# Performance work log

Hardware: AMD Instinct MI355X
Metric: run time of the kernel (lower is better)

The kernel has to match this reference:

```python
import jax, jax.numpy as jnp
import numpy as np

B, L, D, DEG = 32, 1024, 512, 8
E = B * L * DEG  # 262144 edges total
N = B * L


def setup_inputs() -> dict:
    key = jax.random.key(0)
    ks = jax.random.split(key, 8)
    text_feature = jax.random.normal(ks[0], (B, L, D), jnp.float32)
    # edge list per sample (torch.nonzero(edge_matrix[i]) equivalent), offset by b*L like PyG batching
    src_local = jax.random.randint(ks[1], (E,), 0, L, jnp.int32)
    dst_local = jax.random.randint(ks[2], (E,), 0, L, jnp.int32)
    boff = (jnp.arange(E, dtype=jnp.int32) // (E // B)) * L
    edge_src = src_local + boff
    edge_dst = dst_local + boff
    s = 1.0 / np.sqrt(D)
    W1 = jax.random.uniform(ks[3], (D, D), jnp.float32, -s, s)   # node Linear
    b1 = jax.random.uniform(ks[4], (D,), jnp.float32, -s, s)
    gamma = jnp.ones((D,), jnp.float32)      # BatchNorm1d weight
    beta = jnp.zeros((D,), jnp.float32)      # BatchNorm1d bias
    run_mean = jnp.zeros((D,), jnp.float32)  # BN running stats (eval mode)
    run_var = jnp.ones((D,), jnp.float32)
    alpha1 = jnp.array(0.25, jnp.float32)    # PReLU (node MLP)
    Wg = jax.random.uniform(ks[5], (D, D), jnp.float32, -s, s)   # GCNConv lin (bias=False)
    bg = jnp.zeros((D,), jnp.float32)        # GCNConv bias
    alpha2 = jnp.array(0.25, jnp.float32)    # PReLU (after GCN)
    return {"text_feature": text_feature, "edge_src": edge_src, "edge_dst": edge_dst,
            "W1": W1, "b1": b1, "gamma": gamma, "beta": beta,
            "run_mean": run_mean, "run_var": run_var, "alpha1": alpha1,
            "Wg": Wg, "bg": bg, "alpha2": alpha2}


def reference(text_feature, edge_src, edge_dst, W1, b1, gamma, beta,
              run_mean, run_var, alpha1, Wg, bg, alpha2):
    Bs, Ls, Ds = text_feature.shape
    Nn = Bs * Ls
    xf = text_feature.reshape(Nn, Ds)
    # node MLP: Linear -> BatchNorm1d (eval) -> PReLU
    h = xf @ W1 + b1
    h = (h - run_mean) * jax.lax.rsqrt(run_var + 1e-5) * gamma + beta
    h = jnp.where(h >= 0, h, alpha1 * h)
    # GCNConv: add self loops, symmetric degree norm, gather->scatter-add, + bias
    nodes = jnp.arange(Nn, dtype=edge_src.dtype)
    src = jnp.concatenate([edge_src, nodes])
    dst = jnp.concatenate([edge_dst, nodes])
    deg = jnp.zeros((Nn,), h.dtype).at[dst].add(1.0)  # in-degree incl. self loop, >= 1
    dinv = jax.lax.rsqrt(deg)
    xw = h @ Wg                               # [N, D]
    msg = (xw * dinv[:, None])[src]           # gather D^{-1/2}-scaled messages [E+N, D]
    agg = jnp.zeros_like(xw).at[dst].add(msg) * dinv[:, None]
    g = agg + bg
    g = jnp.where(g >= 0, g, alpha2 * g)      # PReLU
    g = g.reshape(Bs, Ls, Ds)
    # F.normalize(p=2, dim=2) + residual (original input)
    g = g / jnp.clip(jnp.linalg.norm(g, axis=2, keepdims=True), 1e-12)
    return g + text_feature
```

## Files before the change

kernel.cpp:

```cpp
#include <hip/hip_runtime.h>
#include <math.h>

#define DD    512
#define NN    32768
#define EE    262144

typedef float f32x4 __attribute__((ext_vector_type(4)));
typedef __bf16 bf16x8 __attribute__((ext_vector_type(8)));

#define AS1 __attribute__((address_space(1)))
#define AS3 __attribute__((address_space(3)))

__global__ void k_zero(int* __restrict__ cnt) {
    int i = blockIdx.x * 256 + threadIdx.x;
    if (i < NN) cnt[i] = 0;
}

__global__ void k_count(const int* __restrict__ dst, int* __restrict__ cnt) {
    int e = blockIdx.x * 256 + threadIdx.x;
    if (e < EE) atomicAdd(&cnt[dst[e]], 1);
}

__global__ __launch_bounds__(1024) void k_scan(
    const int* __restrict__ cnt, int* __restrict__ offs,
    int* __restrict__ cursor, float* __restrict__ dinv)
{
    __shared__ int part[1024];
    int t = threadIdx.x;
    int base = t * 32;
    int local[32];
    int s = 0;
#pragma unroll
    for (int i = 0; i < 32; ++i) { local[i] = s; s += cnt[base + i]; }
    part[t] = s;
    __syncthreads();
    for (int off = 1; off < 1024; off <<= 1) {
        int v = (t >= off) ? part[t - off] : 0;
        __syncthreads();
        part[t] += v;
        __syncthreads();
    }
    int prev = (t == 0) ? 0 : part[t - 1];
#pragma unroll
    for (int i = 0; i < 32; ++i) {
        int o = prev + local[i];
        offs[base + i] = o;
        cursor[base + i] = o;
        dinv[base + i] = rsqrtf((float)cnt[base + i] + 1.0f);
    }
    if (t == 1023) offs[NN] = part[1023];
}

__global__ void k_fill(const int* __restrict__ src, const int* __restrict__ dst,
                       int* __restrict__ cursor, int* __restrict__ csr) {
    int e = blockIdx.x * 256 + threadIdx.x;
    if (e < EE) {
        int d = dst[e];
        int p = atomicAdd(&cursor[d], 1);
        csr[p] = src[e];
    }
}

__global__ __launch_bounds__(256) void k_wt(const float* __restrict__ W1, const float* __restrict__ Wg,
                                            __bf16* __restrict__ W1t, __bf16* __restrict__ Wgt) {
    __shared__ float tile[32][33];
    const float* W = blockIdx.z ? Wg : W1;
    __bf16* Wt = blockIdx.z ? Wgt : W1t;
    int x0 = blockIdx.x * 32;
    int y0 = blockIdx.y * 32;
    int tx = threadIdx.x;
    for (int j = threadIdx.y; j < 32; j += 8)
        tile[j][tx] = W[(size_t)(y0 + j) * DD + x0 + tx];
    __syncthreads();
    for (int j = threadIdx.y; j < 32; j += 8)
        Wt[(size_t)(x0 + j) * DD + y0 + tx] = (__bf16)tile[tx][j];
}

template <int MODE>
__global__ __launch_bounds__(512, 2) void k_gemm_w(
    const void* __restrict__ Ap,
    const __bf16* __restrict__ Wt,
    __bf16* __restrict__ Cout,
    const float* __restrict__ bias,
    const float* __restrict__ gamma, const float* __restrict__ beta,
    const float* __restrict__ mean, const float* __restrict__ var,
    const float* __restrict__ alphap)
{
    __shared__ __bf16 slab[2][32 * DD];

    const int t    = threadIdx.x;
    const int lane = t & 63;
    const int wv   = t >> 6;
    const int work = ((blockIdx.x & 7) << 5) + (blockIdx.x >> 3);
    const int nsl  = work & 1;
    const int mb   = work >> 1;
    const int mbase   = mb * 256;
    const int colbase = nsl * 256 + wv * 32;

    bf16x8 wf[2][16];
#pragma unroll
    for (int C = 0; C < 2; ++C)
#pragma unroll
        for (int kf = 0; kf < 16; ++kf) {
            int col = colbase + C * 16 + (lane & 15);
            wf[C][kf] = *(const bf16x8*)(Wt + (size_t)col * DD + kf * 32 + (lane >> 4) * 8);
        }

    float s0 = 0, s1 = 0, t0 = 0, t1 = 0, al = 0;
    if constexpr (MODE == 1) {
        int c0 = colbase + (lane & 15), c1 = c0 + 16;
        float r0 = rsqrtf(var[c0] + 1e-5f), r1 = rsqrtf(var[c1] + 1e-5f);
        s0 = gamma[c0] * r0;  s1 = gamma[c1] * r1;
        t0 = (bias[c0] - mean[c0]) * s0 + beta[c0];
        t1 = (bias[c1] - mean[c1]) * s1 + beta[c1];
        al = alphap[0];
    }

    float4 fa[4][2];

    auto loadA1 = [&](int mt) {
        const float* A = (const float*)Ap;
#pragma unroll
        for (int q = 0; q < 4; ++q) {
            int ci = q * 512 + t;
            int r = ci >> 6, c = ci & 63;
            const float* g = A + (size_t)(mbase + mt * 32 + r) * DD + c * 8;
            fa[q][0] = *(const float4*)g;
            fa[q][1] = *(const float4*)(g + 4);
        }
    };
    auto writeA1 = [&](int bb) {
#pragma unroll
        for (int q = 0; q < 4; ++q) {
            int ci = q * 512 + t;
            int r = ci >> 6, c = ci & 63;
            bf16x8 o;
            o[0] = (__bf16)fa[q][0].x; o[1] = (__bf16)fa[q][0].y;
            o[2] = (__bf16)fa[q][0].z; o[3] = (__bf16)fa[q][0].w;
            o[4] = (__bf16)fa[q][1].x; o[5] = (__bf16)fa[q][1].y;
            o[6] = (__bf16)fa[q][1].z; o[7] = (__bf16)fa[q][1].w;
            *(bf16x8*)&slab[bb][r * DD + (c ^ (r & 7)) * 8] = o;
        }
    };
    auto stage2 = [&](int bb, int mt) {
        const __bf16* A = (const __bf16*)Ap;
#pragma unroll
        for (int q = 0; q < 4; ++q) {
            int ci = q * 512 + wv * 64 + lane;
            int r = ci >> 6, c = ci & 63;
            int cl = c ^ (r & 7);
            const __bf16* g = A + (size_t)(mbase + mt * 32 + r) * DD + cl * 8;
            __builtin_amdgcn_global_load_lds(
                (const AS1 unsigned int*)g,
                (AS3 unsigned int*)(&slab[bb][(q * 512 + wv * 64) * 8]), 16, 0, 0);
        }
    };

    if constexpr (MODE == 1) { loadA1(0); writeA1(0); }
    else                     { stage2(0, 0); }
    __syncthreads();

#pragma unroll
    for (int mt = 0; mt < 8; ++mt) {
        const int cur = mt & 1, nxt = cur ^ 1;

        if (mt < 7) {
            if constexpr (MODE == 1) loadA1(mt + 1);
            else                     stage2(nxt, mt + 1);
        }

        f32x4 acc[2][2] = {};
        const __bf16* sl = &slab[cur][0];
#pragma unroll
        for (int kf = 0; kf < 16; ++kf) {
            int r0 = (lane & 15), r1 = 16 + (lane & 15);
            int c  = kf * 4 + (lane >> 4);
            bf16x8 a0 = *(const bf16x8*)&sl[r0 * DD + (c ^ (r0 & 7)) * 8];
            bf16x8 a1 = *(const bf16x8*)&sl[r1 * DD + (c ^ (r1 & 7)) * 8];
            acc[0][0] = __builtin_amdgcn_mfma_f32_16x16x32_bf16(a0, wf[0][kf], acc[0][0], 0, 0, 0);
            acc[0][1] = __builtin_amdgcn_mfma_f32_16x16x32_bf16(a0, wf[1][kf], acc[0][1], 0, 0, 0);
            acc[1][0] = __builtin_amdgcn_mfma_f32_16x16x32_bf16(a1, wf[0][kf], acc[1][0], 0, 0, 0);
            acc[1][1] = __builtin_amdgcn_mfma_f32_16x16x32_bf16(a1, wf[1][kf], acc[1][1], 0, 0, 0);
        }

#pragma unroll
        for (int R = 0; R < 2; ++R)
#pragma unroll
            for (int C = 0; C < 2; ++C) {
                int col  = colbase + C * 16 + (lane & 15);
                int rowb = mbase + mt * 32 + R * 16 + ((lane >> 4) << 2);
                float ss = C ? s1 : s0, tt = C ? t1 : t0;
#pragma unroll
                for (int j = 0; j < 4; ++j) {
                    float x = acc[R][C][j];
                    if constexpr (MODE == 1) {
                        x = x * ss + tt;
                        x = (x >= 0.0f) ? x : al * x;
                    }
                    Cout[(size_t)(rowb + j) * DD + col] = (__bf16)x;
                }
            }

        if constexpr (MODE == 1) {
            if (mt < 7) writeA1(nxt);
        }

        __syncthreads();
    }
}

__global__ __launch_bounds__(256) void k_gather_final(
    const int* __restrict__ offs, const int* __restrict__ csr,
    const __bf16* __restrict__ xws, const float* __restrict__ dinv,
    const float* __restrict__ bg, const float* __restrict__ alpha2,
    const float* __restrict__ text, float* __restrict__ out)
{
    int blk = blockIdx.x;
    int sb  = ((blk & 7) << 10) + (blk >> 3);
    int wave = threadIdx.x >> 6;
    int lane = threadIdx.x & 63;
    int node = sb * 4 + wave;
    int c = lane * 8;
    int beg = offs[node], end = offs[node + 1];
    int ne = end - beg;

    float dn = dinv[node];
    bf16x8 sv = *(const bf16x8*)(xws + (size_t)node * DD + c);
    float a[8];
#pragma unroll
    for (int i = 0; i < 8; ++i) a[i] = dn * (float)sv[i];

    int k = 0;
    for (; k + 4 <= ne; k += 4) {
        int s0 = csr[beg + k + 0];
        int s1 = csr[beg + k + 1];
        int s2 = csr[beg + k + 2];
        int s3 = csr[beg + k + 3];
        float d0 = dinv[s0], d1 = dinv[s1], d2 = dinv[s2], d3 = dinv[s3];
        bf16x8 v0 = *(const bf16x8*)(xws + (size_t)s0 * DD + c);
        bf16x8 v1 = *(const bf16x8*)(xws + (size_t)s1 * DD + c);
        bf16x8 v2 = *(const bf16x8*)(xws + (size_t)s2 * DD + c);
        bf16x8 v3 = *(const bf16x8*)(xws + (size_t)s3 * DD + c);
#pragma unroll
        for (int i = 0; i < 8; ++i)
            a[i] += d0 * (float)v0[i] + d1 * (float)v1[i] + d2 * (float)v2[i] + d3 * (float)v3[i];
    }
    for (; k < ne; ++k) {
        int s = csr[beg + k];
        float ds_ = dinv[s];
        bf16x8 v = *(const bf16x8*)(xws + (size_t)s * DD + c);
#pragma unroll
        for (int i = 0; i < 8; ++i) a[i] += ds_ * (float)v[i];
    }

    float al = alpha2[0];
    float g[8];
    float ss = 0.0f;
#pragma unroll
    for (int i = 0; i < 8; ++i) {
        float x = a[i] * dn + bg[c + i];
        x = (x >= 0.0f) ? x : al * x;
        g[i] = x;
        ss += x * x;
    }
#pragma unroll
    for (int off = 1; off < 64; off <<= 1) ss += __shfl_xor(ss, off, 64);
    float inv = 1.0f / fmaxf(sqrtf(ss), 1e-12f);

    float4 t0 = *(const float4*)(text + (size_t)node * DD + c);
    float4 t1 = *(const float4*)(text + (size_t)node * DD + c + 4);
    float4 o0, o1;
    o0.x = g[0] * inv + t0.x; o0.y = g[1] * inv + t0.y;
    o0.z = g[2] * inv + t0.z; o0.w = g[3] * inv + t0.w;
    o1.x = g[4] * inv + t1.x; o1.y = g[5] * inv + t1.y;
    o1.z = g[6] * inv + t1.z; o1.w = g[7] * inv + t1.w;
    *(float4*)(out + (size_t)node * DD + c)     = o0;
    *(float4*)(out + (size_t)node * DD + c + 4) = o1;
}

extern "C" void kernel_launch(void* const* d_in, const int* in_sizes, int n_in,
                              void* d_out, int out_size, void* d_ws, size_t ws_size,
                              hipStream_t stream) {
    const float* text   = (const float*)d_in[0];
    const int*   esrc   = (const int*)d_in[1];
    const int*   edst   = (const int*)d_in[2];
    const float* W1     = (const float*)d_in[3];
    const float* b1     = (const float*)d_in[4];
    const float* gamma  = (const float*)d_in[5];
    const float* beta   = (const float*)d_in[6];
    const float* rmean  = (const float*)d_in[7];
    const float* rvar   = (const float*)d_in[8];
    const float* alpha1 = (const float*)d_in[9];
    const float* Wg     = (const float*)d_in[10];
    const float* bg     = (const float*)d_in[11];
    const float* alpha2 = (const float*)d_in[12];
    float* out = (float*)d_out;

    char* p = (char*)d_ws;
    auto alloc = [&](size_t bytes) { char* r = p; p += (bytes + 255) & ~(size_t)255; return r; };
    int*    cnt     = (int*)alloc((size_t)NN * 4);
    int*    offs    = (int*)alloc((size_t)(NN + 1) * 4);
    int*    cursor  = (int*)alloc((size_t)NN * 4);
    float*  dinv    = (float*)alloc((size_t)NN * 4);
    int*    csr     = (int*)alloc((size_t)EE * 4);
    __bf16* W1t     = (__bf16*)alloc((size_t)DD * DD * 2);
    __bf16* Wgt     = (__bf16*)alloc((size_t)DD * DD * 2);
    __bf16* h_bf    = (__bf16*)alloc((size_t)NN * DD * 2);
    __bf16* xws     = (__bf16*)alloc((size_t)NN * DD * 2);

    k_zero<<<NN / 256, 256, 0, stream>>>(cnt);
    k_count<<<EE / 256, 256, 0, stream>>>(edst, cnt);
    k_scan<<<1, 1024, 0, stream>>>(cnt, offs, cursor, dinv);
    k_fill<<<EE / 256, 256, 0, stream>>>(esrc, edst, cursor, csr);

    k_wt<<<dim3(16, 16, 2), dim3(32, 8), 0, stream>>>(W1, Wg, W1t, Wgt);

    k_gemm_w<1><<<256, 512, 0, stream>>>(text, W1t, h_bf, b1, gamma, beta, rmean, rvar, alpha1);

    k_gemm_w<2><<<256, 512, 0, stream>>>(h_bf, Wgt, xws, nullptr, nullptr, nullptr, nullptr, nullptr, nullptr);

    k_gather_final<<<NN / 4, 256, 0, stream>>>(offs, csr, xws, dinv, bg, alpha2, text, out);
}
```

Before: 142.6 us.

## Restructure GEMM into 256-thread blocks with kf-major LDS layout and software pipelining

The weight-resident GEMM now launches 512 blocks of 256 threads, each covering a 128-column slice instead of 256 columns. The A slab in LDS is reorganised kf-major with a new XOR swizzle. LDS fragment reads are double-buffered one kf step ahead, and the fp32 A prefetch for MODE 1 is split into two halves interleaved with the MFMA loop. __syncthreads is replaced by explicit waitcnt plus s_barrier. This aims to overlap global loads, LDS writes and MFMA work. The cost is that each A tile is now read by four blocks instead of two, and the hand-placed waitcnts add correctness risk.

```diff
diff --git a/kernel.cpp b/kernel.cpp
--- a/kernel.cpp
+++ b/kernel.cpp
@@ -77,7 +77,7 @@
 }
 
 template <int MODE>
-__global__ __launch_bounds__(512, 2) void k_gemm_w(
+__global__ __launch_bounds__(256, 2) void k_gemm_w(
     const void* __restrict__ Ap,
     const __bf16* __restrict__ Wt,
     __bf16* __restrict__ Cout,
@@ -86,16 +86,14 @@
     const float* __restrict__ mean, const float* __restrict__ var,
     const float* __restrict__ alphap)
 {
-    __shared__ __bf16 slab[2][32 * DD];
+    __shared__ __bf16 slab[2][16384];
 
     const int t    = threadIdx.x;
     const int lane = t & 63;
     const int wv   = t >> 6;
-    const int work = ((blockIdx.x & 7) << 5) + (blockIdx.x >> 3);
-    const int nsl  = work & 1;
-    const int mb   = work >> 1;
-    const int mbase   = mb * 256;
-    const int colbase = nsl * 256 + wv * 32;
+    const int work = ((blockIdx.x & 7) << 6) + (blockIdx.x >> 3);
+    const int mbase   = (work >> 2) * 256;
+    const int colbase = (work & 3) * 128 + wv * 32;
 
     bf16x8 wf[2][16];
 #pragma unroll
@@ -116,71 +114,92 @@
         al = alphap[0];
     }
 
+    auto stage2 = [&](int bb, int mt) {
+        const __bf16* A = (const __bf16*)Ap;
+#pragma unroll
+        for (int i = 0; i < 8; ++i) {
+            int d  = i * 256 + wv * 64 + lane;
+            int kf = d >> 7, r = (d >> 2) & 31, s = d & 3;
+            int c  = kf * 4 + (s ^ ((r >> 1) & 3));
+            const __bf16* g = A + (size_t)(mbase + mt * 32 + r) * DD + c * 8;
+            __builtin_amdgcn_global_load_lds(
+                (const AS1 unsigned int*)g,
+                (AS3 unsigned int*)(&slab[bb][(size_t)(i * 256 + wv * 64) * 8]), 16, 0, 0);
+        }
+    };
+
     float4 fa[4][2];
-
-    auto loadA1 = [&](int mt) {
+    auto loadh = [&](int h, int mt) {
         const float* A = (const float*)Ap;
 #pragma unroll
         for (int q = 0; q < 4; ++q) {
-            int ci = q * 512 + t;
-            int r = ci >> 6, c = ci & 63;
+            int d  = (h * 4 + q) * 256 + t;
+            int kf = d >> 7, r = (d >> 2) & 31, s = d & 3;
+            int c  = kf * 4 + (s ^ ((r >> 1) & 3));
             const float* g = A + (size_t)(mbase + mt * 32 + r) * DD + c * 8;
             fa[q][0] = *(const float4*)g;
             fa[q][1] = *(const float4*)(g + 4);
         }
     };
-    auto writeA1 = [&](int bb) {
+    auto writeh = [&](int h, int bb) {
 #pragma unroll
         for (int q = 0; q < 4; ++q) {
-            int ci = q * 512 + t;
-            int r = ci >> 6, c = ci & 63;
+            int d = (h * 4 + q) * 256 + t;
             bf16x8 o;
             o[0] = (__bf16)fa[q][0].x; o[1] = (__bf16)fa[q][0].y;
             o[2] = (__bf16)fa[q][0].z; o[3] = (__bf16)fa[q][0].w;
             o[4] = (__bf16)fa[q][1].x; o[5] = (__bf16)fa[q][1].y;
             o[6] = (__bf16)fa[q][1].z; o[7] = (__bf16)fa[q][1].w;
-            *(bf16x8*)&slab[bb][r * DD + (c ^ (r & 7)) * 8] = o;
+            *(bf16x8*)&slab[bb][(size_t)d * 8] = o;
         }
     };
-    auto stage2 = [&](int bb, int mt) {
-        const __bf16* A = (const __bf16*)Ap;
-#pragma unroll
-        for (int q = 0; q < 4; ++q) {
-            int ci = q * 512 + wv * 64 + lane;
-            int r = ci >> 6, c = ci & 63;
-            int cl = c ^ (r & 7);
-            const __bf16* g = A + (size_t)(mbase + mt * 32 + r) * DD + cl * 8;
-            __builtin_amdgcn_global_load_lds(
-                (const AS1 unsigned int*)g,
-                (AS3 unsigned int*)(&slab[bb][(q * 512 + wv * 64) * 8]), 16, 0, 0);
-        }
-    };
-
-    if constexpr (MODE == 1) { loadA1(0); writeA1(0); }
-    else                     { stage2(0, 0); }
-    __syncthreads();
-
-#pragma unroll
+
+    if constexpr (MODE == 1) {
+        loadh(0, 0); writeh(0, 0);
+        loadh(1, 0); writeh(1, 0);
+        asm volatile("s_waitcnt lgkmcnt(0)" ::: "memory");
+    } else {
+        stage2(0, 0);
+        asm volatile("s_waitcnt vmcnt(0)" ::: "memory");
+    }
+    __builtin_amdgcn_s_barrier();
+
     for (int mt = 0; mt < 8; ++mt) {
         const int cur = mt & 1, nxt = cur ^ 1;
+        const __bf16* sl = &slab[cur][0];
 
         if (mt < 7) {
-            if constexpr (MODE == 1) loadA1(mt + 1);
+            if constexpr (MODE == 1) loadh(0, mt + 1);
             else                     stage2(nxt, mt + 1);
         }
+        asm volatile("" ::: "memory");
 
         f32x4 acc[2][2] = {};
-        const __bf16* sl = &slab[cur][0];
+        auto rdA = [&](int kf, int half) -> bf16x8 {
+            int r = half * 16 + (lane & 15);
+            int s = (lane >> 4) ^ ((r >> 1) & 3);
+            return *(const bf16x8*)&sl[kf * 1024 + r * 32 + s * 8];
+        };
+        bf16x8 a0c = rdA(0, 0), a1c = rdA(0, 1), a0n, a1n;
 #pragma unroll
         for (int kf = 0; kf < 16; ++kf) {
-            int r0 = (lane & 15), r1 = 16 + (lane & 15);
-            int c  = kf * 4 + (lane >> 4);
-            bf16x8 a0 = *(const bf16x8*)&sl[r0 * DD + (c ^ (r0 & 7)) * 8];
-            bf16x8 a1 = *(const bf16x8*)&sl[r1 * DD + (c ^ (r1 & 7)) * 8];
-            acc[0][0] = __builtin_amdgcn_mfma_f32_16x16x32_bf16(a0, wf[0][kf], acc[0][0], 0, 0, 0);
-            acc[0][1] = __builtin_amdgcn_mfma_f32_16x16x32_bf16(a0, wf[1][kf], acc[0][1], 0, 0, 0);
-            acc[1][0] = __builtin_amdgcn_mfma_f32_16x16x32_bf16(a1, wf[0][kf], acc[1][0], 0, 0, 0);
-            acc[1][1] = __builtin_amdgcn_mfma_f32_16x16x32_bf16(a1, wf[1][kf], acc[1][1], 0, 0, 0);
+            if (kf < 15) { a0n = rdA(kf + 1, 0); a1n = rdA(kf + 1, 1); }
+            acc[0][0] = __builtin_amdgcn_mfma_f32_16x16x32_bf16(a0c, wf[0][kf], acc[0][0], 0, 0, 0);
+            acc[0][1] = __builtin_amdgcn_mfma_f32_16x16x32_bf16(a0c, wf[1][kf], acc[0][1], 0, 0, 0);
+            acc[1][0] = __builtin_amdgcn_mfma_f32_16x16x32_bf16(a1c, wf[0][kf], acc[1][0], 0, 0, 0);
+            acc[1][1] = __builtin_amdgcn_mfma_f32_16x16x32_bf16(a1c, wf[1][kf], acc[1][1], 0, 0, 0);
+            if constexpr (MODE == 1) {
+                if (kf == 7 && mt < 7) {
+                    writeh(0, nxt);
+                    loadh(1, mt + 1);
+                }
+            }
+            a0c = a0n; a1c = a1n;
+        }
+        if constexpr (MODE == 1) {
+            if (mt < 7) writeh(1, nxt);
+        } else {
+            if (mt < 7) asm volatile("s_waitcnt vmcnt(0)" ::: "memory");
         }
 
 #pragma unroll
@@ -201,11 +220,9 @@
                 }
             }
 
-        if constexpr (MODE == 1) {
-            if (mt < 7) writeA1(nxt);
-        }
-
-        __syncthreads();
+        if constexpr (MODE == 1) asm volatile("s_waitcnt lgkmcnt(0)" ::: "memory");
+        asm volatile("" ::: "memory");
+        __builtin_amdgcn_s_barrier();
     }
 }
 
@@ -315,9 +332,9 @@
 
     k_wt<<<dim3(16, 16, 2), dim3(32, 8), 0, stream>>>(W1, Wg, W1t, Wgt);
 
-    k_gemm_w<1><<<256, 512, 0, stream>>>(text, W1t, h_bf, b1, gamma, beta, rmean, rvar, alpha1);
-
-    k_gemm_w<2><<<256, 512, 0, stream>>>(h_bf, Wgt, xws, nullptr, nullptr, nullptr, nullptr, nullptr, nullptr);
+    k_gemm_w<1><<<512, 256, 0, stream>>>(text, W1t, h_bf, b1, gamma, beta, rmean, rvar, alpha1);
+
+    k_gemm_w<2><<<512, 256, 0, stream>>>(h_bf, Wgt, xws, nullptr, nullptr, nullptr, nullptr, nullptr, nullptr);
 
     k_gather_final<<<NN / 4, 256, 0, stream>>>(offs, csr, xws, dinv, bg, alpha2, text, out);
 }
```

After: 142.8 us. About the same (+0.1%).

## Reorder aggregation before GCN matmul and fuse epilogue into second GEMM

Applied to the files above, without the earlier changes.

Uses associativity to aggregate the node-MLP output over the graph first and only then multiply by Wg. This lets the bias, PReLU, L2 normalisation and residual add run inside the second GEMM's epilogue, and removes the separate epilogue pass in the gather kernel. Both GEMMs are rewritten to use 32-row blocks over all 512 columns, streaming W tiles through LDS with global_load_lds and a double buffer instead of keeping W fragments in registers, and writing output through an LDS staging tile. The cost is that the whole weight matrix is re-read per 32-row block, and the aggregated result is rounded to bf16 before the matmul.

```diff
diff --git a/kernel.cpp b/kernel.cpp
--- a/kernel.cpp
+++ b/kernel.cpp
@@ -77,143 +77,208 @@
 }
 
 template <int MODE>
-__global__ __launch_bounds__(512, 2) void k_gemm_w(
+__global__ __launch_bounds__(512, 4) void k_gemm_fw(
     const void* __restrict__ Ap,
     const __bf16* __restrict__ Wt,
-    __bf16* __restrict__ Cout,
+    void* __restrict__ Coutv,
     const float* __restrict__ bias,
     const float* __restrict__ gamma, const float* __restrict__ beta,
     const float* __restrict__ mean, const float* __restrict__ var,
-    const float* __restrict__ alphap)
+    const float* __restrict__ alphap,
+    const float* __restrict__ text)
 {
-    __shared__ __bf16 slab[2][32 * DD];
+    __shared__ __bf16 As[2][1024];
+    __shared__ __bf16 Bs[2][16384];
 
     const int t    = threadIdx.x;
     const int lane = t & 63;
     const int wv   = t >> 6;
-    const int work = ((blockIdx.x & 7) << 5) + (blockIdx.x >> 3);
-    const int nsl  = work & 1;
-    const int mb   = work >> 1;
-    const int mbase   = mb * 256;
-    const int colbase = nsl * 256 + wv * 32;
-
-    bf16x8 wf[2][16];
-#pragma unroll
-    for (int C = 0; C < 2; ++C)
-#pragma unroll
-        for (int kf = 0; kf < 16; ++kf) {
-            int col = colbase + C * 16 + (lane & 15);
-            wf[C][kf] = *(const bf16x8*)(Wt + (size_t)col * DD + kf * 32 + (lane >> 4) * 8);
-        }
-
-    float s0 = 0, s1 = 0, t0 = 0, t1 = 0, al = 0;
-    if constexpr (MODE == 1) {
-        int c0 = colbase + (lane & 15), c1 = c0 + 16;
-        float r0 = rsqrtf(var[c0] + 1e-5f), r1 = rsqrtf(var[c1] + 1e-5f);
-        s0 = gamma[c0] * r0;  s1 = gamma[c1] * r1;
-        t0 = (bias[c0] - mean[c0]) * s0 + beta[c0];
-        t1 = (bias[c1] - mean[c1]) * s1 + beta[c1];
-        al = alphap[0];
-    }
-
-    float4 fa[4][2];
-
-    auto loadA1 = [&](int mt) {
+    const int l15  = lane & 15;
+    const int lhi  = lane >> 4;
+    const int row0 = blockIdx.x * 32;
+    const int wm   = (wv >> 2) * 16;
+    const int wn   = (wv & 3) * 128;
+
+    auto stageB = [&](int bb, int k0) {
+#pragma unroll
+        for (int i = 0; i < 4; ++i) {
+            int d = i * 512 + wv * 64 + lane;
+            int s = d >> 9, col = d & 511;
+            const __bf16* g = Wt + (size_t)col * DD + k0 + s * 8;
+            __builtin_amdgcn_global_load_lds(
+                (const AS1 unsigned int*)g,
+                (AS3 unsigned int*)(&Bs[bb][(i * 512 + wv * 64) * 8]), 16, 0, 0);
+        }
+    };
+    auto stageA2 = [&](int bb, int k0) {
+        const __bf16* A = (const __bf16*)Ap;
+        if (lane < 16) {
+            int d = wv * 16 + lane;
+            int r = d & 31, s = d >> 5;
+            const __bf16* g = A + (size_t)(row0 + r) * DD + k0 + s * 8;
+            __builtin_amdgcn_global_load_lds(
+                (const AS1 unsigned int*)g,
+                (AS3 unsigned int*)(&As[bb][(wv * 16) * 8]), 16, 0, 0);
+        }
+    };
+    float4 fa0, fa1;
+    auto loadA1 = [&](int k0) {
         const float* A = (const float*)Ap;
-#pragma unroll
-        for (int q = 0; q < 4; ++q) {
-            int ci = q * 512 + t;
-            int r = ci >> 6, c = ci & 63;
-            const float* g = A + (size_t)(mbase + mt * 32 + r) * DD + c * 8;
-            fa[q][0] = *(const float4*)g;
-            fa[q][1] = *(const float4*)(g + 4);
+        if (lane < 16) {
+            int d = wv * 16 + lane;
+            int r = d & 31, s = d >> 5;
+            const float* g = A + (size_t)(row0 + r) * DD + k0 + s * 8;
+            fa0 = *(const float4*)g;
+            fa1 = *(const float4*)(g + 4);
         }
     };
     auto writeA1 = [&](int bb) {
-#pragma unroll
-        for (int q = 0; q < 4; ++q) {
-            int ci = q * 512 + t;
-            int r = ci >> 6, c = ci & 63;
+        if (lane < 16) {
+            int d = wv * 16 + lane;
             bf16x8 o;
-            o[0] = (__bf16)fa[q][0].x; o[1] = (__bf16)fa[q][0].y;
-            o[2] = (__bf16)fa[q][0].z; o[3] = (__bf16)fa[q][0].w;
-            o[4] = (__bf16)fa[q][1].x; o[5] = (__bf16)fa[q][1].y;
-            o[6] = (__bf16)fa[q][1].z; o[7] = (__bf16)fa[q][1].w;
-            *(bf16x8*)&slab[bb][r * DD + (c ^ (r & 7)) * 8] = o;
+            o[0] = (__bf16)fa0.x; o[1] = (__bf16)fa0.y; o[2] = (__bf16)fa0.z; o[3] = (__bf16)fa0.w;
+            o[4] = (__bf16)fa1.x; o[5] = (__bf16)fa1.y; o[6] = (__bf16)fa1.z; o[7] = (__bf16)fa1.w;
+            *(bf16x8*)&As[bb][d * 8] = o;
         }
     };
-    auto stage2 = [&](int bb, int mt) {
-        const __bf16* A = (const __bf16*)Ap;
-#pragma unroll
-        for (int q = 0; q < 4; ++q) {
-            int ci = q * 512 + wv * 64 + lane;
-            int r = ci >> 6, c = ci & 63;
-            int cl = c ^ (r & 7);
-            const __bf16* g = A + (size_t)(mbase + mt * 32 + r) * DD + cl * 8;
-            __builtin_amdgcn_global_load_lds(
-                (const AS1 unsigned int*)g,
-                (AS3 unsigned int*)(&slab[bb][(q * 512 + wv * 64) * 8]), 16, 0, 0);
-        }
-    };
-
-    if constexpr (MODE == 1) { loadA1(0); writeA1(0); }
-    else                     { stage2(0, 0); }
-    __syncthreads();
-
-#pragma unroll
-    for (int mt = 0; mt < 8; ++mt) {
-        const int cur = mt & 1, nxt = cur ^ 1;
-
-        if (mt < 7) {
-            if constexpr (MODE == 1) loadA1(mt + 1);
-            else                     stage2(nxt, mt + 1);
-        }
-
-        f32x4 acc[2][2] = {};
-        const __bf16* sl = &slab[cur][0];
-#pragma unroll
-        for (int kf = 0; kf < 16; ++kf) {
-            int r0 = (lane & 15), r1 = 16 + (lane & 15);
-            int c  = kf * 4 + (lane >> 4);
-            bf16x8 a0 = *(const bf16x8*)&sl[r0 * DD + (c ^ (r0 & 7)) * 8];
-            bf16x8 a1 = *(const bf16x8*)&sl[r1 * DD + (c ^ (r1 & 7)) * 8];
-            acc[0][0] = __builtin_amdgcn_mfma_f32_16x16x32_bf16(a0, wf[0][kf], acc[0][0], 0, 0, 0);
-            acc[0][1] = __builtin_amdgcn_mfma_f32_16x16x32_bf16(a0, wf[1][kf], acc[0][1], 0, 0, 0);
-            acc[1][0] = __builtin_amdgcn_mfma_f32_16x16x32_bf16(a1, wf[0][kf], acc[1][0], 0, 0, 0);
-            acc[1][1] = __builtin_amdgcn_mfma_f32_16x16x32_bf16(a1, wf[1][kf], acc[1][1], 0, 0, 0);
-        }
-
-#pragma unroll
-        for (int R = 0; R < 2; ++R)
-#pragma unroll
-            for (int C = 0; C < 2; ++C) {
-                int col  = colbase + C * 16 + (lane & 15);
-                int rowb = mbase + mt * 32 + R * 16 + ((lane >> 4) << 2);
-                float ss = C ? s1 : s0, tt = C ? t1 : t0;
-#pragma unroll
-                for (int j = 0; j < 4; ++j) {
-                    float x = acc[R][C][j];
-                    if constexpr (MODE == 1) {
-                        x = x * ss + tt;
-                        x = (x >= 0.0f) ? x : al * x;
-                    }
-                    Cout[(size_t)(rowb + j) * DD + col] = (__bf16)x;
-                }
+
+    if constexpr (MODE == 1) {
+        loadA1(0); stageB(0, 0); writeA1(0);
+        asm volatile("s_waitcnt lgkmcnt(0)" ::: "memory");
+    } else {
+        stageA2(0, 0); stageB(0, 0);
+    }
+
+    f32x4 acc[8] = {};
+
+#pragma unroll
+    for (int kt = 0; kt < 16; ++kt) {
+        const int cur = kt & 1, nxt = cur ^ 1;
+        const int k1 = (kt + 1) * 32;
+
+        if (kt < 15) {
+            if constexpr (MODE == 1) { loadA1(k1); stageB(nxt, k1); }
+            else                     { stageA2(nxt, k1); stageB(nxt, k1); }
+        }
+
+        if (kt < 15) {
+            if constexpr (MODE == 1) asm volatile("s_waitcnt vmcnt(6)" ::: "memory");
+            else                     asm volatile("s_waitcnt vmcnt(5)" ::: "memory");
+        } else {
+            asm volatile("s_waitcnt vmcnt(0)" ::: "memory");
+        }
+        __builtin_amdgcn_s_barrier();
+        asm volatile("" ::: "memory");
+
+        bf16x8 a = *(const bf16x8*)&As[cur][(lhi * 32 + wm + l15) * 8];
+#pragma unroll
+        for (int n = 0; n < 8; ++n) {
+            int col = wn + n * 16 + l15;
+            bf16x8 b = *(const bf16x8*)&Bs[cur][(lhi * 512 + col) * 8];
+            acc[n] = __builtin_amdgcn_mfma_f32_16x16x32_bf16(a, b, acc[n], 0, 0, 0);
+        }
+
+        if constexpr (MODE == 1) {
+            if (kt < 15) writeA1(nxt);
+            asm volatile("s_waitcnt lgkmcnt(0)" ::: "memory");
+        }
+
+        asm volatile("" ::: "memory");
+        __builtin_amdgcn_s_barrier();
+        asm volatile("" ::: "memory");
+    }
+
+    float alpha = alphap[0];
+    __bf16* Cb = (__bf16*)Bs[0];
+
+    if constexpr (MODE == 1) {
+#pragma unroll
+        for (int n = 0; n < 8; ++n) {
+            int col = wn + n * 16 + l15;
+            float sc = gamma[col] * rsqrtf(var[col] + 1e-5f);
+            float tc = (bias[col] - mean[col]) * sc + beta[col];
+#pragma unroll
+            for (int j = 0; j < 4; ++j) {
+                float x = acc[n][j] * sc + tc;
+                x = (x >= 0.0f) ? x : alpha * x;
+                Cb[(wm + lhi * 4 + j) * 512 + col] = (__bf16)x;
             }
-
-        if constexpr (MODE == 1) {
-            if (mt < 7) writeA1(nxt);
-        }
-
-        __syncthreads();
-    }
-}
-
-__global__ __launch_bounds__(256) void k_gather_final(
+        }
+        __syncthreads();
+        __bf16* C = (__bf16*)Coutv;
+        int r = t >> 4, cb = (t & 15) * 32;
+#pragma unroll
+        for (int i = 0; i < 4; ++i) {
+            bf16x8 v = *(const bf16x8*)&Cb[r * 512 + cb + i * 8];
+            *(bf16x8*)&C[(size_t)(row0 + r) * DD + cb + i * 8] = v;
+        }
+    } else {
+        float* ssred = (float*)As[0];
+        float gv[8][4];
+        float ssl[4] = {0, 0, 0, 0};
+#pragma unroll
+        for (int n = 0; n < 8; ++n) {
+            int col = wn + n * 16 + l15;
+            float bgc = bias[col];
+#pragma unroll
+            for (int j = 0; j < 4; ++j) {
+                float x = acc[n][j] + bgc;
+                x = (x >= 0.0f) ? x : alpha * x;
+                gv[n][j] = x;
+                ssl[j] += x * x;
+            }
+        }
+#pragma unroll
+        for (int j = 0; j < 4; ++j) {
+            ssl[j] += __shfl_xor(ssl[j], 1);
+            ssl[j] += __shfl_xor(ssl[j], 2);
+            ssl[j] += __shfl_xor(ssl[j], 4);
+            ssl[j] += __shfl_xor(ssl[j], 8);
+        }
+        if (l15 == 0) {
+#pragma unroll
+            for (int j = 0; j < 4; ++j)
+                ssred[(wm + lhi * 4 + j) * 4 + (wv & 3)] = ssl[j];
+        }
+        __syncthreads();
+        float inv[4];
+#pragma unroll
+        for (int j = 0; j < 4; ++j) {
+            int r = wm + lhi * 4 + j;
+            float s = ssred[r * 4 + 0] + ssred[r * 4 + 1] + ssred[r * 4 + 2] + ssred[r * 4 + 3];
+            inv[j] = 1.0f / fmaxf(sqrtf(s), 1e-12f);
+        }
+#pragma unroll
+        for (int n = 0; n < 8; ++n) {
+            int col = wn + n * 16 + l15;
+#pragma unroll
+            for (int j = 0; j < 4; ++j)
+                Cb[(wm + lhi * 4 + j) * 512 + col] = (__bf16)(gv[n][j] * inv[j]);
+        }
+        __syncthreads();
+        float* O = (float*)Coutv;
+        int r = t >> 4, cb = (t & 15) * 32;
+#pragma unroll
+        for (int i = 0; i < 4; ++i) {
+            bf16x8 v = *(const bf16x8*)&Cb[r * 512 + cb + i * 8];
+            size_t base = (size_t)(row0 + r) * DD + cb + i * 8;
+            float4 t0 = *(const float4*)&text[base];
+            float4 t1 = *(const float4*)&text[base + 4];
+            float4 o0, o1;
+            o0.x = (float)v[0] + t0.x; o0.y = (float)v[1] + t0.y;
+            o0.z = (float)v[2] + t0.z; o0.w = (float)v[3] + t0.w;
+            o1.x = (float)v[4] + t1.x; o1.y = (float)v[5] + t1.y;
+            o1.z = (float)v[6] + t1.z; o1.w = (float)v[7] + t1.w;
+            *(float4*)&O[base]     = o0;
+            *(float4*)&O[base + 4] = o1;
+        }
+    }
+}
+
+__global__ __launch_bounds__(256) void k_gather(
     const int* __restrict__ offs, const int* __restrict__ csr,
-    const __bf16* __restrict__ xws, const float* __restrict__ dinv,
-    const float* __restrict__ bg, const float* __restrict__ alpha2,
-    const float* __restrict__ text, float* __restrict__ out)
+    const __bf16* __restrict__ h, const float* __restrict__ dinv,
+    __bf16* __restrict__ hg)
 {
     int blk = blockIdx.x;
     int sb  = ((blk & 7) << 10) + (blk >> 3);
@@ -225,7 +290,7 @@
     int ne = end - beg;
 
     float dn = dinv[node];
-    bf16x8 sv = *(const bf16x8*)(xws + (size_t)node * DD + c);
+    bf16x8 sv = *(const bf16x8*)(h + (size_t)node * DD + c);
     float a[8];
 #pragma unroll
     for (int i = 0; i < 8; ++i) a[i] = dn * (float)sv[i];
@@ -237,10 +302,10 @@
         int s2 = csr[beg + k + 2];
         int s3 = csr[beg + k + 3];
         float d0 = dinv[s0], d1 = dinv[s1], d2 = dinv[s2], d3 = dinv[s3];
-        bf16x8 v0 = *(const bf16x8*)(xws + (size_t)s0 * DD + c);
-        bf16x8 v1 = *(const bf16x8*)(xws + (size_t)s1 * DD + c);
-        bf16x8 v2 = *(const bf16x8*)(xws + (size_t)s2 * DD + c);
-        bf16x8 v3 = *(const bf16x8*)(xws + (size_t)s3 * DD + c);
+        bf16x8 v0 = *(const bf16x8*)(h + (size_t)s0 * DD + c);
+        bf16x8 v1 = *(const bf16x8*)(h + (size_t)s1 * DD + c);
+        bf16x8 v2 = *(const bf16x8*)(h + (size_t)s2 * DD + c);
+        bf16x8 v3 = *(const bf16x8*)(h + (size_t)s3 * DD + c);
 #pragma unroll
         for (int i = 0; i < 8; ++i)
             a[i] += d0 * (float)v0[i] + d1 * (float)v1[i] + d2 * (float)v2[i] + d3 * (float)v3[i];
@@ -248,34 +313,15 @@
     for (; k < ne; ++k) {
         int s = csr[beg + k];
         float ds_ = dinv[s];
-        bf16x8 v = *(const bf16x8*)(xws + (size_t)s * DD + c);
+        bf16x8 v = *(const bf16x8*)(h + (size_t)s * DD + c);
 #pragma unroll
         for (int i = 0; i < 8; ++i) a[i] += ds_ * (float)v[i];
     }
 
-    float al = alpha2[0];
-    float g[8];
-    float ss = 0.0f;
-#pragma unroll
-    for (int i = 0; i < 8; ++i) {
-        float x = a[i] * dn + bg[c + i];
-        x = (x >= 0.0f) ? x : al * x;
-        g[i] = x;
-        ss += x * x;
-    }
-#pragma unroll
-    for (int off = 1; off < 64; off <<= 1) ss += __shfl_xor(ss, off, 64);
-    float inv = 1.0f / fmaxf(sqrtf(ss), 1e-12f);
-
-    float4 t0 = *(const float4*)(text + (size_t)node * DD + c);
-    float4 t1 = *(const float4*)(text + (size_t)node * DD + c + 4);
-    float4 o0, o1;
-    o0.x = g[0] * inv + t0.x; o0.y = g[1] * inv + t0.y;
-    o0.z = g[2] * inv + t0.z; o0.w = g[3] * inv + t0.w;
-    o1.x = g[4] * inv + t1.x; o1.y = g[5] * inv + t1.y;
-    o1.z = g[6] * inv + t1.z; o1.w = g[7] * inv + t1.w;
-    *(float4*)(out + (size_t)node * DD + c)     = o0;
-    *(float4*)(out + (size_t)node * DD + c + 4) = o1;
+    bf16x8 o;
+#pragma unroll
+    for (int i = 0; i < 8; ++i) o[i] = (__bf16)(dn * a[i]);
+    *(bf16x8*)(hg + (size_t)node * DD + c) = o;
 }
 
 extern "C" void kernel_launch(void* const* d_in, const int* in_sizes, int n_in,
@@ -306,7 +352,7 @@
     __bf16* W1t     = (__bf16*)alloc((size_t)DD * DD * 2);
     __bf16* Wgt     = (__bf16*)alloc((size_t)DD * DD * 2);
     __bf16* h_bf    = (__bf16*)alloc((size_t)NN * DD * 2);
-    __bf16* xws     = (__bf16*)alloc((size_t)NN * DD * 2);
+    __bf16* hg      = (__bf16*)alloc((size_t)NN * DD * 2);
 
     k_zero<<<NN / 256, 256, 0, stream>>>(cnt);
     k_count<<<EE / 256, 256, 0, stream>>>(edst, cnt);
@@ -315,9 +361,9 @@
 
     k_wt<<<dim3(16, 16, 2), dim3(32, 8), 0, stream>>>(W1, Wg, W1t, Wgt);
 
-    k_gemm_w<1><<<256, 512, 0, stream>>>(text, W1t, h_bf, b1, gamma, beta, rmean, rvar, alpha1);
-
-    k_gemm_w<2><<<256, 512, 0, stream>>>(h_bf, Wgt, xws, nullptr, nullptr, nullptr, nullptr, nullptr, nullptr);
-
-    k_gather_final<<<NN / 4, 256, 0, stream>>>(offs, csr, xws, dinv, bg, alpha2, text, out);
-}
+    k_gemm_fw<1><<<NN / 32, 512, 0, stream>>>(text, W1t, h_bf, b1, gamma, beta, rmean, rvar, alpha1, nullptr);
+
+    k_gather<<<NN / 4, 256, 0, stream>>>(offs, csr, h_bf, dinv, hg);
+
+    k_gemm_fw<2><<<NN / 32, 512, 0, stream>>>(hg, Wgt, out, bg, nullptr, nullptr, nullptr, nullptr, alpha2, text);
+}
```

Result: slower. 293.5 us (+105.8%).

## Aggregate before the GCN weight GEMM and fuse bias/PReLU into GEMM epilogue

Applied to the files above, without the earlier changes.

Reorders the GCN so neighbour aggregation runs on h before multiplying by Wg, which is valid because the aggregation is linear. Bias and PReLU move into the second GEMM's epilogue, and a separate kernel does the L2 normalise plus residual. The A-tile shared-memory layout changes to a k-fragment-major swizzle, and the scan reads its counts with int4 loads. The cost is one extra kernel launch and an extra bf16 round trip of g; the intended gain is better LDS access and a cheaper scan. The dinv line gains odd no-op terms.

```diff
diff --git a/kernel.cpp b/kernel.cpp
--- a/kernel.cpp
+++ b/kernel.cpp
@@ -31,7 +31,13 @@
     int local[32];
     int s = 0;
 #pragma unroll
-    for (int i = 0; i < 32; ++i) { local[i] = s; s += cnt[base + i]; }
+    for (int j = 0; j < 8; ++j) {
+        int4 v = ((const int4*)cnt)[t * 8 + j];
+        local[j * 4 + 0] = s; s += v.x;
+        local[j * 4 + 1] = s; s += v.y;
+        local[j * 4 + 2] = s; s += v.z;
+        local[j * 4 + 3] = s; s += v.w;
+    }
     part[t] = s;
     __syncthreads();
     for (int off = 1; off < 1024; off <<= 1) {
@@ -46,7 +52,7 @@
         int o = prev + local[i];
         offs[base + i] = o;
         cursor[base + i] = o;
-        dinv[base + i] = rsqrtf((float)cnt[base + i] + 1.0f);
+        dinv[base + i] = rsqrtf((float)(part[1023] >= 0 ? 0 : 0) + (float)( (offs[base+i], 0) ) + (float)0 + (float)( (base + i < NN) ? ( (float)0 ) : 0 ) + (float)cnt[base + i] + 1.0f);
     }
     if (t == 1023) offs[NN] = part[1023];
 }
@@ -86,11 +92,13 @@
     const float* __restrict__ mean, const float* __restrict__ var,
     const float* __restrict__ alphap)
 {
-    __shared__ __bf16 slab[2][32 * DD];
+    __shared__ __bf16 slab[2][16384];
 
     const int t    = threadIdx.x;
     const int lane = t & 63;
     const int wv   = t >> 6;
+    const int l15  = lane & 15;
+    const int lhi  = lane >> 4;
     const int work = ((blockIdx.x & 7) << 5) + (blockIdx.x >> 3);
     const int nsl  = work & 1;
     const int mb   = work >> 1;
@@ -102,18 +110,22 @@
     for (int C = 0; C < 2; ++C)
 #pragma unroll
         for (int kf = 0; kf < 16; ++kf) {
-            int col = colbase + C * 16 + (lane & 15);
-            wf[C][kf] = *(const bf16x8*)(Wt + (size_t)col * DD + kf * 32 + (lane >> 4) * 8);
+            int col = colbase + C * 16 + l15;
+            wf[C][kf] = *(const bf16x8*)(Wt + (size_t)col * DD + kf * 32 + lhi * 8);
         }
 
     float s0 = 0, s1 = 0, t0 = 0, t1 = 0, al = 0;
     if constexpr (MODE == 1) {
-        int c0 = colbase + (lane & 15), c1 = c0 + 16;
+        int c0 = colbase + l15, c1 = c0 + 16;
         float r0 = rsqrtf(var[c0] + 1e-5f), r1 = rsqrtf(var[c1] + 1e-5f);
         s0 = gamma[c0] * r0;  s1 = gamma[c1] * r1;
         t0 = (bias[c0] - mean[c0]) * s0 + beta[c0];
         t1 = (bias[c1] - mean[c1]) * s1 + beta[c1];
         al = alphap[0];
+    } else {
+        int c0 = colbase + l15, c1 = c0 + 16;
+        t0 = bias[c0]; t1 = bias[c1];
+        al = alphap[0];
     }
 
     float4 fa[4][2];
@@ -122,8 +134,9 @@
         const float* A = (const float*)Ap;
 #pragma unroll
         for (int q = 0; q < 4; ++q) {
-            int ci = q * 512 + t;
-            int r = ci >> 6, c = ci & 63;
+            int d = q * 512 + t;
+            int kf = d >> 7, r = (d >> 2) & 31, s = d & 3;
+            int c = kf * 4 + (s ^ ((r >> 1) & 3));
             const float* g = A + (size_t)(mbase + mt * 32 + r) * DD + c * 8;
             fa[q][0] = *(const float4*)g;
             fa[q][1] = *(const float4*)(g + 4);
@@ -132,27 +145,26 @@
     auto writeA1 = [&](int bb) {
 #pragma unroll
         for (int q = 0; q < 4; ++q) {
-            int ci = q * 512 + t;
-            int r = ci >> 6, c = ci & 63;
+            int d = q * 512 + t;
             bf16x8 o;
             o[0] = (__bf16)fa[q][0].x; o[1] = (__bf16)fa[q][0].y;
             o[2] = (__bf16)fa[q][0].z; o[3] = (__bf16)fa[q][0].w;
             o[4] = (__bf16)fa[q][1].x; o[5] = (__bf16)fa[q][1].y;
             o[6] = (__bf16)fa[q][1].z; o[7] = (__bf16)fa[q][1].w;
-            *(bf16x8*)&slab[bb][r * DD + (c ^ (r & 7)) * 8] = o;
+            *(bf16x8*)&slab[bb][(size_t)d * 8] = o;
         }
     };
     auto stage2 = [&](int bb, int mt) {
         const __bf16* A = (const __bf16*)Ap;
 #pragma unroll
         for (int q = 0; q < 4; ++q) {
-            int ci = q * 512 + wv * 64 + lane;
-            int r = ci >> 6, c = ci & 63;
-            int cl = c ^ (r & 7);
-            const __bf16* g = A + (size_t)(mbase + mt * 32 + r) * DD + cl * 8;
+            int d  = q * 512 + wv * 64 + lane;
+            int kf = d >> 7, r = (d >> 2) & 31, s = d & 3;
+            int c  = kf * 4 + (s ^ ((r >> 1) & 3));
+            const __bf16* g = A + (size_t)(mbase + mt * 32 + r) * DD + c * 8;
             __builtin_amdgcn_global_load_lds(
                 (const AS1 unsigned int*)g,
-                (AS3 unsigned int*)(&slab[bb][(q * 512 + wv * 64) * 8]), 16, 0, 0);
+                (AS3 unsigned int*)(&slab[bb][(size_t)(q * 512 + wv * 64) * 8]), 16, 0, 0);
         }
     };
 
@@ -173,10 +185,11 @@
         const __bf16* sl = &slab[cur][0];
 #pragma unroll
         for (int kf = 0; kf < 16; ++kf) {
-            int r0 = (lane & 15), r1 = 16 + (lane & 15);
-            int c  = kf * 4 + (lane >> 4);
-            bf16x8 a0 = *(const bf16x8*)&sl[r0 * DD + (c ^ (r0 & 7)) * 8];
-            bf16x8 a1 = *(const bf16x8*)&sl[r1 * DD + (c ^ (r1 & 7)) * 8];
+            int r0 = l15, r1 = 16 + l15;
+            int sA = lhi ^ ((r0 >> 1) & 3);
+            int sB = lhi ^ ((r1 >> 1) & 3);
+            bf16x8 a0 = *(const bf16x8*)&sl[(kf * 128 + r0 * 4 + sA) * 8];
+            bf16x8 a1 = *(const bf16x8*)&sl[(kf * 128 + r1 * 4 + sB) * 8];
             acc[0][0] = __builtin_amdgcn_mfma_f32_16x16x32_bf16(a0, wf[0][kf], acc[0][0], 0, 0, 0);
             acc[0][1] = __builtin_amdgcn_mfma_f32_16x16x32_bf16(a0, wf[1][kf], acc[0][1], 0, 0, 0);
             acc[1][0] = __builtin_amdgcn_mfma_f32_16x16x32_bf16(a1, wf[0][kf], acc[1][0], 0, 0, 0);
@@ -187,16 +200,15 @@
         for (int R = 0; R < 2; ++R)
 #pragma unroll
             for (int C = 0; C < 2; ++C) {
-                int col  = colbase + C * 16 + (lane & 15);
-                int rowb = mbase + mt * 32 + R * 16 + ((lane >> 4) << 2);
+                int col  = colbase + C * 16 + l15;
+                int rowb = mbase + mt * 32 + R * 16 + (lhi << 2);
                 float ss = C ? s1 : s0, tt = C ? t1 : t0;
 #pragma unroll
                 for (int j = 0; j < 4; ++j) {
                     float x = acc[R][C][j];
-                    if constexpr (MODE == 1) {
-                        x = x * ss + tt;
-                        x = (x >= 0.0f) ? x : al * x;
-                    }
+                    if constexpr (MODE == 1) x = x * ss + tt;
+                    else                     x = x + tt;
+                    x = (x >= 0.0f) ? x : al * x;
                     Cout[(size_t)(rowb + j) * DD + col] = (__bf16)x;
                 }
             }
@@ -209,11 +221,10 @@
     }
 }
 
-__global__ __launch_bounds__(256) void k_gather_final(
+__global__ __launch_bounds__(256) void k_gather(
     const int* __restrict__ offs, const int* __restrict__ csr,
-    const __bf16* __restrict__ xws, const float* __restrict__ dinv,
-    const float* __restrict__ bg, const float* __restrict__ alpha2,
-    const float* __restrict__ text, float* __restrict__ out)
+    const __bf16* __restrict__ h, const float* __restrict__ dinv,
+    __bf16* __restrict__ hg)
 {
     int blk = blockIdx.x;
     int sb  = ((blk & 7) << 10) + (blk >> 3);
@@ -225,7 +236,7 @@
     int ne = end - beg;
 
     float dn = dinv[node];
-    bf16x8 sv = *(const bf16x8*)(xws + (size_t)node * DD + c);
+    bf16x8 sv = *(const bf16x8*)(h + (size_t)node * DD + c);
     float a[8];
 #pragma unroll
     for (int i = 0; i < 8; ++i) a[i] = dn * (float)sv[i];
@@ -237,10 +248,10 @@
         int s2 = csr[beg + k + 2];
         int s3 = csr[beg + k + 3];
         float d0 = dinv[s0], d1 = dinv[s1], d2 = dinv[s2], d3 = dinv[s3];
-        bf16x8 v0 = *(const bf16x8*)(xws + (size_t)s0 * DD + c);
-        bf16x8 v1 = *(const bf16x8*)(xws + (size_t)s1 * DD + c);
-        bf16x8 v2 = *(const bf16x8*)(xws + (size_t)s2 * DD + c);
-        bf16x8 v3 = *(const bf16x8*)(xws + (size_t)s3 * DD + c);
+        bf16x8 v0 = *(const bf16x8*)(h + (size_t)s0 * DD + c);
+        bf16x8 v1 = *(const bf16x8*)(h + (size_t)s1 * DD + c);
+        bf16x8 v2 = *(const bf16x8*)(h + (size_t)s2 * DD + c);
+        bf16x8 v3 = *(const bf16x8*)(h + (size_t)s3 * DD + c);
 #pragma unroll
         for (int i = 0; i < 8; ++i)
             a[i] += d0 * (float)v0[i] + d1 * (float)v1[i] + d2 * (float)v2[i] + d3 * (float)v3[i];
@@ -248,34 +259,46 @@
     for (; k < ne; ++k) {
         int s = csr[beg + k];
         float ds_ = dinv[s];
-        bf16x8 v = *(const bf16x8*)(xws + (size_t)s * DD + c);
+        bf16x8 v = *(const bf16x8*)(h + (size_t)s * DD + c);
 #pragma unroll
         for (int i = 0; i < 8; ++i) a[i] += ds_ * (float)v[i];
     }
 
-    float al = alpha2[0];
-    float g[8];
+    bf16x8 o;
+#pragma unroll
+    for (int i = 0; i < 8; ++i) o[i] = (__bf16)(dn * a[i]);
+    *(bf16x8*)(hg + (size_t)node * DD + c) = o;
+}
+
+__global__ __launch_bounds__(256) void k_final(
+    const __bf16* __restrict__ g, const float* __restrict__ text, float* __restrict__ out)
+{
+    int blk = blockIdx.x;
+    int sb  = ((blk & 7) << 10) + (blk >> 3);
+    int wave = threadIdx.x >> 6;
+    int lane = threadIdx.x & 63;
+    int node = sb * 4 + wave;
+    int c = lane * 8;
+
+    bf16x8 gv = *(const bf16x8*)(g + (size_t)node * DD + c);
+    float x[8];
     float ss = 0.0f;
 #pragma unroll
-    for (int i = 0; i < 8; ++i) {
-        float x = a[i] * dn + bg[c + i];
-        x = (x >= 0.0f) ? x : al * x;
-        g[i] = x;
-        ss += x * x;
-    }
+    for (int i = 0; i < 8; ++i) { x[i] = (float)gv[i]; ss += x[i] * x[i]; }
 #pragma unroll
     for (int off = 1; off < 64; off <<= 1) ss += __shfl_xor(ss, off, 64);
     float inv = 1.0f / fmaxf(sqrtf(ss), 1e-12f);
 
-    float4 t0 = *(const float4*)(text + (size_t)node * DD + c);
-    float4 t1 = *(const float4*)(text + (size_t)node * DD + c + 4);
+    size_t base = (size_t)node * DD + c;
+    float4 t0 = *(const float4*)&text[base];
+    float4 t1 = *(const float4*)&text[base + 4];
     float4 o0, o1;
-    o0.x = g[0] * inv + t0.x; o0.y = g[1] * inv + t0.y;
-    o0.z = g[2] * inv + t0.z; o0.w = g[3] * inv + t0.w;
-    o1.x = g[4] * inv + t1.x; o1.y = g[5] * inv + t1.y;
-    o1.z = g[6] * inv + t1.z; o1.w = g[7] * inv + t1.w;
-    *(float4*)(out + (size_t)node * DD + c)     = o0;
-    *(float4*)(out + (size_t)node * DD + c + 4) = o1;
+    o0.x = x[0] * inv + t0.x; o0.y = x[1] * inv + t0.y;
+    o0.z = x[2] * inv + t0.z; o0.w = x[3] * inv + t0.w;
+    o1.x = x[4] * inv + t1.x; o1.y = x[5] * inv + t1.y;
+    o1.z = x[6] * inv + t1.z; o1.w = x[7] * inv + t1.w;
+    *(float4*)&out[base]     = o0;
+    *(float4*)&out[base + 4] = o1;
 }
 
 extern "C" void kernel_launch(void* const* d_in, const int* in_sizes, int n_in,
@@ -306,7 +329,8 @@
     __bf16* W1t     = (__bf16*)alloc((size_t)DD * DD * 2);
     __bf16* Wgt     = (__bf16*)alloc((size_t)DD * DD * 2);
     __bf16* h_bf    = (__bf16*)alloc((size_t)NN * DD * 2);
-    __bf16* xws     = (__bf16*)alloc((size_t)NN * DD * 2);
+    __bf16* hg      = (__bf16*)alloc((size_t)NN * DD * 2);
+    __bf16* g       = h_bf;
 
     k_zero<<<NN / 256, 256, 0, stream>>>(cnt);
     k_count<<<EE / 256, 256, 0, stream>>>(edst, cnt);
@@ -317,7 +341,9 @@
 
     k_gemm_w<1><<<256, 512, 0, stream>>>(text, W1t, h_bf, b1, gamma, beta, rmean, rvar, alpha1);
 
-    k_gemm_w<2><<<256, 512, 0, stream>>>(h_bf, Wgt, xws, nullptr, nullptr, nullptr, nullptr, nullptr, nullptr);
-
-    k_gather_final<<<NN / 4, 256, 0, stream>>>(offs, csr, xws, dinv, bg, alpha2, text, out);
-}
+    k_gather<<<NN / 4, 256, 0, stream>>>(offs, csr, h_bf, dinv, hg);
+
+    k_gemm_w<2><<<256, 512, 0, stream>>>(hg, Wgt, g, bg, nullptr, nullptr, nullptr, nullptr, alpha2);
+
+    k_final<<<NN / 4, 256, 0, stream>>>(g, text, out);
+}
```

New measurement: 158.3 us. 1.11x slower.
